# Kernel tuning notes

Hardware: AMD Instinct MI355X
Metric: run time of the kernel (lower is better)

## Reference

```python
import jax, jax.numpy as jnp
import numpy as np

DIM, EMBED, HEADS = 768, 512, 8
HEAD_DIM = EMBED // HEADS


def setup_inputs() -> dict:
    key = jax.random.key(0)
    ks = jax.random.split(key, 11)
    B, S = 4, 2048
    s = 0.02
    return {
        "query": jax.random.normal(ks[0], (B, S, DIM), jnp.float32),
        "key": jax.random.normal(ks[1], (B, S, DIM), jnp.float32),
        "value": jax.random.normal(ks[2], (B, S, DIM), jnp.float32),
        "wq": jax.random.normal(ks[3], (DIM, EMBED), jnp.float32) * s,
        "bq": jnp.zeros((EMBED,), jnp.float32),
        "wk": jax.random.normal(ks[4], (DIM, EMBED), jnp.float32) * s,
        "bk": jnp.zeros((EMBED,), jnp.float32),
        "wv": jax.random.normal(ks[5], (DIM, EMBED), jnp.float32) * s,
        "bv": jnp.zeros((EMBED,), jnp.float32),
        "wo": jax.random.normal(ks[6], (EMBED, DIM), jnp.float32) * s,
        "bo": jnp.zeros((DIM,), jnp.float32),
    }


def reference(query, key, value, wq, bq, wk, bk, wv, bv, wo, bo):
    B, S, _ = query.shape
    # QKV projections -> [B, H, S, Dh]
    def split_heads(x):
        return x.reshape(B, -1, HEADS, HEAD_DIM).transpose(0, 2, 1, 3)
    q = split_heads(query @ wq + bq)
    k = split_heads(key @ wk + bk)
    v = split_heads(value @ wv + bv)
    scores = jnp.einsum("bhqd,bhkd->bhqk", q, k) / jnp.sqrt(jnp.float32(HEAD_DIM))
    p = jax.nn.softmax(scores, axis=-1)
    x = jnp.einsum("bhqk,bhkd->bhqd", p, v)
    x = x.transpose(0, 2, 1, 3).reshape(B, S, EMBED)
    return x @ wo + bo
```

## Files before the change

### kernel.cpp

```cpp
#include <hip/hip_runtime.h>
#include <math.h>

#define NH   8
#define HD   64
#define BS   4
#define SEQL 2048
#define DIMX 768
#define EMB  512
#define MROWS (BS*SEQL)
#define NSPLIT 2
#define KSPAN (SEQL/NSPLIT)

typedef __attribute__((ext_vector_type(4))) float          f32x4;
typedef __attribute__((ext_vector_type(8))) __bf16         bf16x8;
typedef __attribute__((ext_vector_type(8))) unsigned short u16x8;
typedef __attribute__((ext_vector_type(4))) unsigned short u16x4;

union BF8 { u16x8 u; bf16x8 b; };

__device__ __forceinline__ unsigned short f2bf(float x) {
    unsigned int u = __float_as_uint(x);
    u += 0x7FFFu + ((u >> 16) & 1u);
    return (unsigned short)(u >> 16);
}

#if __has_builtin(__builtin_amdgcn_exp2f)
#define EXP2F(x) __builtin_amdgcn_exp2f(x)
#else
#define EXP2F(x) exp2f(x)
#endif

__device__ __forceinline__ bf16x8 ldb8(const unsigned short* p) {
    return *(const bf16x8*)p;
}

__global__ __launch_bounds__(256)
void cast3(const float* __restrict__ q, const float* __restrict__ k,
           const float* __restrict__ v, unsigned short* __restrict__ out)
{
    const float* src = blockIdx.y == 0 ? q : (blockIdx.y == 1 ? k : v);
    unsigned short* dst = out + (size_t)blockIdx.y * (MROWS * DIMX);
    const int n4 = MROWS * DIMX / 4;
    for (int i = blockIdx.x * 256 + threadIdx.x; i < n4; i += gridDim.x * 256) {
        f32x4 x = ((const f32x4*)src)[i];
        u16x4 o;
        o[0] = f2bf(x[0]); o[1] = f2bf(x[1]); o[2] = f2bf(x[2]); o[3] = f2bf(x[3]);
        ((u16x4*)dst)[i] = o;
    }
}

__global__ __launch_bounds__(256)
void transpose_w4(const float* __restrict__ w0, const float* __restrict__ w1,
                  const float* __restrict__ w2, const float* __restrict__ w3,
                  unsigned short* __restrict__ o0, unsigned short* __restrict__ o1,
                  unsigned short* __restrict__ o2, unsigned short* __restrict__ o3)
{
    __shared__ float sm[32][33];
    const int which = blockIdx.y;
    const float* in; unsigned short* out; int R, C;
    if      (which == 0) { in = w0; out = o0; R = DIMX; C = EMB;  }
    else if (which == 1) { in = w1; out = o1; R = DIMX; C = EMB;  }
    else if (which == 2) { in = w2; out = o2; R = DIMX; C = EMB;  }
    else                 { in = w3; out = o3; R = EMB;  C = DIMX; }
    const int nbx = C / 32;
    const int rB = (blockIdx.x / nbx) * 32, cB = (blockIdx.x % nbx) * 32;
    const int row = threadIdx.x >> 3, c4 = (threadIdx.x & 7) * 4;
    f32x4 v = *(const f32x4*)&in[(size_t)(rB + row) * C + cB + c4];
    sm[row][c4 + 0] = v[0]; sm[row][c4 + 1] = v[1];
    sm[row][c4 + 2] = v[2]; sm[row][c4 + 3] = v[3];
    __syncthreads();
    u16x4 o;
    o[0] = f2bf(sm[c4 + 0][row]); o[1] = f2bf(sm[c4 + 1][row]);
    o[2] = f2bf(sm[c4 + 2][row]); o[3] = f2bf(sm[c4 + 3][row]);
    *(u16x4*)&out[(size_t)(cB + row) * R + rB + c4] = o;
}

template<bool DIRECT>
__device__ __forceinline__ void gemm_core(
    const unsigned short* __restrict__ A, const unsigned short* __restrict__ Bt,
    int K, int mBase, int nBase,
    unsigned short* __restrict__ smA, unsigned short* __restrict__ smB,
    f32x4 (&acc)[4][4])
{
    const int tid = threadIdx.x;
    const int lane = tid & 63, w = tid >> 6;
    const int quad = lane >> 4, lanem = lane & 15;
    const int wm = w >> 1, wn = w & 1;
    const int srow = tid >> 3, c8 = (tid & 7) * 8;

    const f32x4 z4 = {0.f, 0.f, 0.f, 0.f};
    #pragma unroll
    for (int i = 0; i < 4; ++i)
        #pragma unroll
        for (int j = 0; j < 4; ++j) acc[i][j] = z4;

    for (int k0 = 0; k0 < K; k0 += 64) {
        u16x8 va[4], vb[4];
        #pragma unroll
        for (int p = 0; p < 4; ++p) {
            va[p] = *(const u16x8*)&A[(size_t)(mBase + srow + p * 32) * K + k0 + c8];
            vb[p] = *(const u16x8*)&Bt[(size_t)(nBase + srow + p * 32) * K + k0 + c8];
        }
        __syncthreads();
        #pragma unroll
        for (int p = 0; p < 4; ++p) {
            *(u16x8*)&smA[(srow + p * 32) * 72 + c8] = va[p];
            *(u16x8*)&smB[(srow + p * 32) * 72 + c8] = vb[p];
        }
        __syncthreads();
        #pragma unroll
        for (int kk = 0; kk < 64; kk += 32) {
            bf16x8 xa[4], wb[4];
            #pragma unroll
            for (int mt = 0; mt < 4; ++mt)
                xa[mt] = ldb8(&smA[(wm * 64 + mt * 16 + lanem) * 72 + kk + quad * 8]);
            #pragma unroll
            for (int nt = 0; nt < 4; ++nt)
                wb[nt] = ldb8(&smB[(wn * 64 + nt * 16 + lanem) * 72 + kk + quad * 8]);
            if constexpr (DIRECT) {
                #pragma unroll
                for (int mt = 0; mt < 4; ++mt)
                    #pragma unroll
                    for (int nt = 0; nt < 4; ++nt)
                        acc[mt][nt] = __builtin_amdgcn_mfma_f32_16x16x32_bf16(xa[mt], wb[nt], acc[mt][nt], 0, 0, 0);
            } else {
                #pragma unroll
                for (int nt = 0; nt < 4; ++nt)
                    #pragma unroll
                    for (int mt = 0; mt < 4; ++mt)
                        acc[nt][mt] = __builtin_amdgcn_mfma_f32_16x16x32_bf16(wb[nt], xa[mt], acc[nt][mt], 0, 0, 0);
            }
        }
    }
}

__global__ __launch_bounds__(256)
void gemm_qkv(const unsigned short* __restrict__ Xc, const unsigned short* __restrict__ Wt,
              const float* __restrict__ bq, const float* __restrict__ bk,
              const float* __restrict__ bv,
              unsigned short* __restrict__ Qb, unsigned short* __restrict__ Kb,
              unsigned short* __restrict__ Vtb)
{
    __shared__ unsigned short smA[128 * 72];
    __shared__ unsigned short smB[128 * 72];
    const int z = blockIdx.z;
    const unsigned short* A  = Xc + (size_t)z * (MROWS * DIMX);
    const unsigned short* Bt = Wt + (size_t)z * (EMB * DIMX);
    const float* bias = z == 0 ? bq : (z == 1 ? bk : bv);
    const int mBase = blockIdx.y * 128, nBase = blockIdx.x * 128;

    const int tid = threadIdx.x;
    const int lane = tid & 63, w = tid >> 6;
    const int quad = lane >> 4, lanem = lane & 15;
    const int wm = w >> 1, wn = w & 1;

    f32x4 acc[4][4];
    if (z == 2) {
        gemm_core<true>(A, Bt, DIMX, mBase, nBase, smA, smB, acc);
        #pragma unroll
        for (int mt = 0; mt < 4; ++mt) {
            const int sg = mBase + wm * 64 + mt * 16 + quad * 4;
            const int b = sg >> 11, s = sg & 2047;
            #pragma unroll
            for (int nt = 0; nt < 4; ++nt) {
                const int de = nBase + wn * 64 + nt * 16 + lanem;
                const float bvv = bias[de];
                const int h = de >> 6, dh = de & 63;
                u16x4 ov;
                #pragma unroll
                for (int r = 0; r < 4; ++r) ov[r] = f2bf(acc[mt][nt][r] + bvv);
                *(u16x4*)&Vtb[((size_t)((b * NH + h) * HD + dh) << 11) + s] = ov;
            }
        }
    } else {
        gemm_core<false>(A, Bt, DIMX, mBase, nBase, smA, smB, acc);
        const float os = (z == 0) ? 0.18033688f : 1.0f;
        unsigned short* C = (z == 0) ? Qb : Kb;
        #pragma unroll
        for (int nt = 0; nt < 4; ++nt) {
            const int n0 = nBase + wn * 64 + nt * 16 + quad * 4;
            const f32x4 b4 = *(const f32x4*)&bias[n0];
            #pragma unroll
            for (int mt = 0; mt < 4; ++mt) {
                const int m = mBase + wm * 64 + mt * 16 + lanem;
                u16x4 ov;
                #pragma unroll
                for (int r = 0; r < 4; ++r) ov[r] = f2bf((acc[nt][mt][r] + b4[r]) * os);
                *(u16x4*)&C[(size_t)m * EMB + n0] = ov;
            }
        }
    }
}

__global__ __launch_bounds__(256)
void gemm_out(const unsigned short* __restrict__ Xb, const unsigned short* __restrict__ Wot,
              const float* __restrict__ bo, float* __restrict__ out)
{
    __shared__ unsigned short smA[128 * 72];
    __shared__ unsigned short smB[128 * 72];
    const int mBase = blockIdx.y * 128, nBase = blockIdx.x * 128;
    const int tid = threadIdx.x;
    const int lane = tid & 63, w = tid >> 6;
    const int quad = lane >> 4, lanem = lane & 15;
    const int wm = w >> 1, wn = w & 1;

    f32x4 acc[4][4];
    gemm_core<false>(Xb, Wot, EMB, mBase, nBase, smA, smB, acc);
    #pragma unroll
    for (int nt = 0; nt < 4; ++nt) {
        const int n0 = nBase + wn * 64 + nt * 16 + quad * 4;
        const f32x4 b4 = *(const f32x4*)&bo[n0];
        #pragma unroll
        for (int mt = 0; mt < 4; ++mt) {
            const int m = mBase + wm * 64 + mt * 16 + lanem;
            f32x4 ov = acc[nt][mt] + b4;
            *(f32x4*)&out[(size_t)m * DIMX + n0] = ov;
        }
    }
}

__global__ __launch_bounds__(256)
void attn_mfma(const unsigned short* __restrict__ Qb, const unsigned short* __restrict__ Kb,
               const unsigned short* __restrict__ Vt,
               float* __restrict__ Opart, float* __restrict__ lpart)
{
    __shared__ unsigned short smK[64 * 72];
    __shared__ unsigned short smV[64 * 72];
    __shared__ unsigned short smP[4][32 * 72];
    const int id = blockIdx.x;
    const int bh = ((id & 7) << 2) | ((id >> 3) & 3);
    const int rest = id >> 5;
    const int qb = rest & 15, sp = rest >> 4;
    const int b = bh >> 3, h = bh & 7;

    const int tid = threadIdx.x;
    const int w = tid >> 6, lane = tid & 63;
    const int quad = lane >> 4, lanem = lane & 15;

    bf16x8 aq[2][2];
    #pragma unroll
    for (int rg = 0; rg < 2; ++rg) {
        const size_t qrow = (size_t)(b * SEQL + qb * 128 + w * 32 + rg * 16 + lanem) * EMB + h * HD;
        aq[rg][0] = ldb8(&Qb[qrow + quad * 8]);
        aq[rg][1] = ldb8(&Qb[qrow + 32 + quad * 8]);
    }

    const f32x4 z4 = {0.f, 0.f, 0.f, 0.f};
    f32x4 o[4][2];
    f32x4 ls[2] = {z4, z4};
    #pragma unroll
    for (int dt = 0; dt < 4; ++dt)
        #pragma unroll
        for (int rg = 0; rg < 2; ++rg) o[dt][rg] = z4;

    BF8 ones;
    #pragma unroll
    for (int i = 0; i < 8; ++i) ones.u[i] = 0x3F80;

    const unsigned short* Kbase = Kb + (size_t)b * SEQL * EMB + h * HD;
    const unsigned short* Vbase = Vt + (size_t)bh * HD * SEQL;
    unsigned short* pW = &smP[w][0];
    const int srow = tid >> 3, c8 = (tid & 7) * 8;

    for (int t = 0; t < KSPAN / 64; ++t) {
        const int k0 = sp * KSPAN + t * 64;
        u16x8 kv[2], vv[2];
        #pragma unroll
        for (int p = 0; p < 2; ++p) {
            kv[p] = *(const u16x8*)&Kbase[(size_t)(k0 + srow + p * 32) * EMB + c8];
            vv[p] = *(const u16x8*)&Vbase[(size_t)(srow + p * 32) * SEQL + k0 + c8];
        }
        __syncthreads();
        #pragma unroll
        for (int p = 0; p < 2; ++p) {
            *(u16x8*)&smK[(srow + p * 32) * 72 + c8] = kv[p];
            *(u16x8*)&smV[(srow + p * 32) * 72 + c8] = vv[p];
        }
        __syncthreads();

        #pragma unroll
        for (int nt = 0; nt < 4; ++nt) {
            bf16x8 bk0 = ldb8(&smK[(nt * 16 + lanem) * 72 + quad * 8]);
            bf16x8 bk1 = ldb8(&smK[(nt * 16 + lanem) * 72 + 32 + quad * 8]);
            #pragma unroll
            for (int rg = 0; rg < 2; ++rg) {
                f32x4 s = __builtin_amdgcn_mfma_f32_16x16x32_bf16(bk0, aq[rg][0], z4, 0, 0, 0);
                s = __builtin_amdgcn_mfma_f32_16x16x32_bf16(bk1, aq[rg][1], s, 0, 0, 0);
                u16x4 pk;
                #pragma unroll
                for (int r = 0; r < 4; ++r)
                    pk[r] = (unsigned short)(__float_as_uint(EXP2F(s[r])) >> 16);
                *(u16x4*)&pW[(rg * 16 + lanem) * 72 + nt * 16 + quad * 4] = pk;
            }
        }
        bf16x8 pb[2][2];
        #pragma unroll
        for (int rg = 0; rg < 2; ++rg) {
            pb[rg][0] = ldb8(&pW[(rg * 16 + lanem) * 72 + quad * 8]);
            pb[rg][1] = ldb8(&pW[(rg * 16 + lanem) * 72 + 32 + quad * 8]);
        }
        #pragma unroll
        for (int dt = 0; dt < 4; ++dt) {
            bf16x8 av0 = ldb8(&smV[(dt * 16 + lanem) * 72 + quad * 8]);
            bf16x8 av1 = ldb8(&smV[(dt * 16 + lanem) * 72 + 32 + quad * 8]);
            #pragma unroll
            for (int rg = 0; rg < 2; ++rg) {
                o[dt][rg] = __builtin_amdgcn_mfma_f32_16x16x32_bf16(av0, pb[rg][0], o[dt][rg], 0, 0, 0);
                o[dt][rg] = __builtin_amdgcn_mfma_f32_16x16x32_bf16(av1, pb[rg][1], o[dt][rg], 0, 0, 0);
            }
        }
        #pragma unroll
        for (int rg = 0; rg < 2; ++rg) {
            ls[rg] = __builtin_amdgcn_mfma_f32_16x16x32_bf16(ones.b, pb[rg][0], ls[rg], 0, 0, 0);
            ls[rg] = __builtin_amdgcn_mfma_f32_16x16x32_bf16(ones.b, pb[rg][1], ls[rg], 0, 0, 0);
        }
    }

    #pragma unroll
    for (int rg = 0; rg < 2; ++rg) {
        const int qloc = qb * 128 + w * 32 + rg * 16 + lanem;
        float* orow = Opart + ((size_t)sp * 32 * SEQL + (size_t)bh * SEQL + qloc) * HD;
        #pragma unroll
        for (int dt = 0; dt < 4; ++dt)
            *(f32x4*)&orow[dt * 16 + quad * 4] = o[dt][rg];
        if (quad == 0)
            lpart[(size_t)sp * 32 * SEQL + (size_t)bh * SEQL + qloc] = ls[rg][0];
    }
}

__global__ __launch_bounds__(256)
void attn_reduce(const float* __restrict__ Opart, const float* __restrict__ lpart,
                 unsigned short* __restrict__ Xb)
{
    const int lin = blockIdx.x * 256 + threadIdx.x;
    const int d4 = (lin & 15) << 2;
    const int q = (lin >> 4) & 2047;
    const int bh = lin >> 15;
    const int b = bh >> 3, h = bh & 7;
    const size_t base = ((size_t)bh * SEQL + q) * HD + d4;
    const size_t soff = (size_t)32 * SEQL * HD;
    f32x4 o0 = *(const f32x4*)&Opart[base];
    f32x4 o1 = *(const f32x4*)&Opart[base + soff];
    const float l0 = lpart[(size_t)bh * SEQL + q];
    const float l1 = lpart[(size_t)32 * SEQL + (size_t)bh * SEQL + q];
    const float rl = 1.f / (l0 + l1);
    u16x4 ov;
    #pragma unroll
    for (int r = 0; r < 4; ++r) ov[r] = f2bf((o0[r] + o1[r]) * rl);
    *(u16x4*)&Xb[((size_t)(b * SEQL + q)) * EMB + h * HD + d4] = ov;
}

extern "C" void kernel_launch(void* const* d_in, const int* in_sizes, int n_in,
                              void* d_out, int out_size, void* d_ws, size_t ws_size,
                              hipStream_t stream) {
    (void)in_sizes; (void)n_in; (void)out_size; (void)ws_size;
    const float* query = (const float*)d_in[0];
    const float* key   = (const float*)d_in[1];
    const float* value = (const float*)d_in[2];
    const float* wq = (const float*)d_in[3];
    const float* bq = (const float*)d_in[4];
    const float* wk = (const float*)d_in[5];
    const float* bk = (const float*)d_in[6];
    const float* wv = (const float*)d_in[7];
    const float* bv = (const float*)d_in[8];
    const float* wo = (const float*)d_in[9];
    const float* bo = (const float*)d_in[10];
    float* out = (float*)d_out;

    char* ws = (char*)d_ws;
    unsigned short* castb = (unsigned short*)(ws);
    float*          Opart = (float*)(ws);
    float*          lpart = (float*)(ws + 33554432);
    unsigned short* Wt    = (unsigned short*)(ws + 37748736);
    unsigned short* Wot   = (unsigned short*)(ws + 40108032);
    unsigned short* Qbuf  = (unsigned short*)(ws + 40894464);
    unsigned short* Xbuf  = Qbuf;
    unsigned short* Kbuf  = (unsigned short*)(ws + 49283072);
    unsigned short* Vtb   = (unsigned short*)(ws + 57671680);

    const dim3 blk(256);

    transpose_w4<<<dim3(384, 4), blk, 0, stream>>>(wq, wk, wv, wo,
        Wt, Wt + (size_t)EMB * DIMX, Wt + 2 * (size_t)EMB * DIMX, Wot);
    cast3<<<dim3(1024, 3), blk, 0, stream>>>(query, key, value, castb);

    gemm_qkv<<<dim3(EMB / 128, MROWS / 128, 3), blk, 0, stream>>>(
        castb, Wt, bq, bk, bv, Qbuf, Kbuf, Vtb);

    attn_mfma<<<dim3(32 * 16 * NSPLIT), blk, 0, stream>>>(Qbuf, Kbuf, Vtb, Opart, lpart);
    attn_reduce<<<dim3(4096), blk, 0, stream>>>(Opart, lpart, Xbuf);

    gemm_out<<<dim3(DIMX / 128, MROWS / 128), blk, 0, stream>>>(Xbuf, Wot, bo, out);
}
```

Baseline: 247.6 us.

## Fuse input cast into QKV GEMM, prefetch tiles, bf16 partials, 4-way KV split

Removes the separate fp32-to-bf16 cast kernel: the QKV GEMM now loads fp32 activations directly and packs them to bf16 by truncation with a byte-permute. The GEMM and attention loops register-prefetch the next tile while computing the current one. Attention partial outputs are stored as bf16 instead of fp32, and the KV split rises from 2 to 4 for more parallelism, with the reduce kernel summing all splits. Trade-offs are more register pressure, truncation instead of round-to-nearest on inputs, lower precision in the partial sums, and extra reduce traffic from the larger split.

Result: slower. 286.3 us (+15.6%).

```diff
diff --git a/kernel.cpp b/kernel.cpp
--- a/kernel.cpp
+++ b/kernel.cpp
@@ -8,7 +8,7 @@
 #define DIMX 768
 #define EMB  512
 #define MROWS (BS*SEQL)
-#define NSPLIT 2
+#define NSPLIT 4
 #define KSPAN (SEQL/NSPLIT)
 
 typedef __attribute__((ext_vector_type(4))) float          f32x4;
@@ -22,6 +22,10 @@
     unsigned int u = __float_as_uint(x);
     u += 0x7FFFu + ((u >> 16) & 1u);
     return (unsigned short)(u >> 16);
+}
+
+__device__ __forceinline__ unsigned int pktrunc(float a, float b) {
+    return __builtin_amdgcn_perm(__float_as_uint(b), __float_as_uint(a), 0x07060302);
 }
 
 #if __has_builtin(__builtin_amdgcn_exp2f)
@@ -32,21 +36,6 @@
 
 __device__ __forceinline__ bf16x8 ldb8(const unsigned short* p) {
     return *(const bf16x8*)p;
-}
-
-__global__ __launch_bounds__(256)
-void cast3(const float* __restrict__ q, const float* __restrict__ k,
-           const float* __restrict__ v, unsigned short* __restrict__ out)
-{
-    const float* src = blockIdx.y == 0 ? q : (blockIdx.y == 1 ? k : v);
-    unsigned short* dst = out + (size_t)blockIdx.y * (MROWS * DIMX);
-    const int n4 = MROWS * DIMX / 4;
-    for (int i = blockIdx.x * 256 + threadIdx.x; i < n4; i += gridDim.x * 256) {
-        f32x4 x = ((const f32x4*)src)[i];
-        u16x4 o;
-        o[0] = f2bf(x[0]); o[1] = f2bf(x[1]); o[2] = f2bf(x[2]); o[3] = f2bf(x[3]);
-        ((u16x4*)dst)[i] = o;
-    }
 }
 
 __global__ __launch_bounds__(256)
@@ -75,9 +64,9 @@
     *(u16x4*)&out[(size_t)(cB + row) * R + rB + c4] = o;
 }
 
-template<bool DIRECT>
+template<bool DIRECT, bool AF32>
 __device__ __forceinline__ void gemm_core(
-    const unsigned short* __restrict__ A, const unsigned short* __restrict__ Bt,
+    const void* __restrict__ Av, const unsigned short* __restrict__ Bt,
     int K, int mBase, int nBase,
     unsigned short* __restrict__ smA, unsigned short* __restrict__ smB,
     f32x4 (&acc)[4][4])
@@ -87,6 +76,8 @@
     const int quad = lane >> 4, lanem = lane & 15;
     const int wm = w >> 1, wn = w & 1;
     const int srow = tid >> 3, c8 = (tid & 7) * 8;
+    const unsigned short* Ab = (const unsigned short*)Av;
+    const float* Af = (const float*)Av;
 
     const f32x4 z4 = {0.f, 0.f, 0.f, 0.f};
     #pragma unroll
@@ -94,13 +85,30 @@
         #pragma unroll
         for (int j = 0; j < 4; ++j) acc[i][j] = z4;
 
+    auto ldA = [&](int p, int k0) -> u16x8 {
+        if constexpr (AF32) {
+            const float* bp = &Af[(size_t)(mBase + srow + p * 32) * K + k0 + c8];
+            f32x4 x0 = *(const f32x4*)bp;
+            f32x4 x1 = *(const f32x4*)(bp + 4);
+            union { unsigned int d[4]; u16x8 u; } t;
+            t.d[0] = pktrunc(x0[0], x0[1]);
+            t.d[1] = pktrunc(x0[2], x0[3]);
+            t.d[2] = pktrunc(x1[0], x1[1]);
+            t.d[3] = pktrunc(x1[2], x1[3]);
+            return t.u;
+        } else {
+            return *(const u16x8*)&Ab[(size_t)(mBase + srow + p * 32) * K + k0 + c8];
+        }
+    };
+    auto ldB = [&](int p, int k0) -> u16x8 {
+        return *(const u16x8*)&Bt[(size_t)(nBase + srow + p * 32) * K + k0 + c8];
+    };
+
+    u16x8 va[4], vb[4];
+    #pragma unroll
+    for (int p = 0; p < 4; ++p) { va[p] = ldA(p, 0); vb[p] = ldB(p, 0); }
+
     for (int k0 = 0; k0 < K; k0 += 64) {
-        u16x8 va[4], vb[4];
-        #pragma unroll
-        for (int p = 0; p < 4; ++p) {
-            va[p] = *(const u16x8*)&A[(size_t)(mBase + srow + p * 32) * K + k0 + c8];
-            vb[p] = *(const u16x8*)&Bt[(size_t)(nBase + srow + p * 32) * K + k0 + c8];
-        }
         __syncthreads();
         #pragma unroll
         for (int p = 0; p < 4; ++p) {
@@ -108,6 +116,10 @@
             *(u16x8*)&smB[(srow + p * 32) * 72 + c8] = vb[p];
         }
         __syncthreads();
+        const int kn = (k0 + 64 < K) ? k0 + 64 : 0;
+        #pragma unroll
+        for (int p = 0; p < 4; ++p) { va[p] = ldA(p, kn); vb[p] = ldB(p, kn); }
+
         #pragma unroll
         for (int kk = 0; kk < 64; kk += 32) {
             bf16x8 xa[4], wb[4];
@@ -135,7 +147,8 @@
 }
 
 __global__ __launch_bounds__(256)
-void gemm_qkv(const unsigned short* __restrict__ Xc, const unsigned short* __restrict__ Wt,
+void gemm_qkv(const float* __restrict__ query, const float* __restrict__ keyt,
+              const float* __restrict__ value, const unsigned short* __restrict__ Wt,
               const float* __restrict__ bq, const float* __restrict__ bk,
               const float* __restrict__ bv,
               unsigned short* __restrict__ Qb, unsigned short* __restrict__ Kb,
@@ -144,7 +157,7 @@
     __shared__ unsigned short smA[128 * 72];
     __shared__ unsigned short smB[128 * 72];
     const int z = blockIdx.z;
-    const unsigned short* A  = Xc + (size_t)z * (MROWS * DIMX);
+    const float* A = z == 0 ? query : (z == 1 ? keyt : value);
     const unsigned short* Bt = Wt + (size_t)z * (EMB * DIMX);
     const float* bias = z == 0 ? bq : (z == 1 ? bk : bv);
     const int mBase = blockIdx.y * 128, nBase = blockIdx.x * 128;
@@ -156,7 +169,7 @@
 
     f32x4 acc[4][4];
     if (z == 2) {
-        gemm_core<true>(A, Bt, DIMX, mBase, nBase, smA, smB, acc);
+        gemm_core<true, true>(A, Bt, DIMX, mBase, nBase, smA, smB, acc);
         #pragma unroll
         for (int mt = 0; mt < 4; ++mt) {
             const int sg = mBase + wm * 64 + mt * 16 + quad * 4;
@@ -173,7 +186,7 @@
             }
         }
     } else {
-        gemm_core<false>(A, Bt, DIMX, mBase, nBase, smA, smB, acc);
+        gemm_core<false, true>(A, Bt, DIMX, mBase, nBase, smA, smB, acc);
         const float os = (z == 0) ? 0.18033688f : 1.0f;
         unsigned short* C = (z == 0) ? Qb : Kb;
         #pragma unroll
@@ -205,7 +218,7 @@
     const int wm = w >> 1, wn = w & 1;
 
     f32x4 acc[4][4];
-    gemm_core<false>(Xb, Wot, EMB, mBase, nBase, smA, smB, acc);
+    gemm_core<false, false>(Xb, Wot, EMB, mBase, nBase, smA, smB, acc);
     #pragma unroll
     for (int nt = 0; nt < 4; ++nt) {
         const int n0 = nBase + wn * 64 + nt * 16 + quad * 4;
@@ -222,7 +235,7 @@
 __global__ __launch_bounds__(256)
 void attn_mfma(const unsigned short* __restrict__ Qb, const unsigned short* __restrict__ Kb,
                const unsigned short* __restrict__ Vt,
-               float* __restrict__ Opart, float* __restrict__ lpart)
+               unsigned short* __restrict__ Opart, float* __restrict__ lpart)
 {
     __shared__ unsigned short smK[64 * 72];
     __shared__ unsigned short smV[64 * 72];
@@ -262,14 +275,14 @@
     unsigned short* pW = &smP[w][0];
     const int srow = tid >> 3, c8 = (tid & 7) * 8;
 
+    u16x8 kv[2], vv[2];
+    #pragma unroll
+    for (int p = 0; p < 2; ++p) {
+        kv[p] = *(const u16x8*)&Kbase[(size_t)(sp * KSPAN + srow + p * 32) * EMB + c8];
+        vv[p] = *(const u16x8*)&Vbase[(size_t)(srow + p * 32) * SEQL + sp * KSPAN + c8];
+    }
+
     for (int t = 0; t < KSPAN / 64; ++t) {
-        const int k0 = sp * KSPAN + t * 64;
-        u16x8 kv[2], vv[2];
-        #pragma unroll
-        for (int p = 0; p < 2; ++p) {
-            kv[p] = *(const u16x8*)&Kbase[(size_t)(k0 + srow + p * 32) * EMB + c8];
-            vv[p] = *(const u16x8*)&Vbase[(size_t)(srow + p * 32) * SEQL + k0 + c8];
-        }
         __syncthreads();
         #pragma unroll
         for (int p = 0; p < 2; ++p) {
@@ -277,6 +290,12 @@
             *(u16x8*)&smV[(srow + p * 32) * 72 + c8] = vv[p];
         }
         __syncthreads();
+        const int k1 = (t + 1 < KSPAN / 64) ? sp * KSPAN + (t + 1) * 64 : sp * KSPAN;
+        #pragma unroll
+        for (int p = 0; p < 2; ++p) {
+            kv[p] = *(const u16x8*)&Kbase[(size_t)(k1 + srow + p * 32) * EMB + c8];
+            vv[p] = *(const u16x8*)&Vbase[(size_t)(srow + p * 32) * SEQL + k1 + c8];
+        }
 
         #pragma unroll
         for (int nt = 0; nt < 4; ++nt) {
@@ -319,17 +338,22 @@
     #pragma unroll
     for (int rg = 0; rg < 2; ++rg) {
         const int qloc = qb * 128 + w * 32 + rg * 16 + lanem;
-        float* orow = Opart + ((size_t)sp * 32 * SEQL + (size_t)bh * SEQL + qloc) * HD;
-        #pragma unroll
-        for (int dt = 0; dt < 4; ++dt)
-            *(f32x4*)&orow[dt * 16 + quad * 4] = o[dt][rg];
+        unsigned short* orow =
+            Opart + ((size_t)sp * 32 * SEQL + (size_t)bh * SEQL + qloc) * HD;
+        #pragma unroll
+        for (int dt = 0; dt < 4; ++dt) {
+            u16x4 ov;
+            #pragma unroll
+            for (int r = 0; r < 4; ++r) ov[r] = f2bf(o[dt][rg][r]);
+            *(u16x4*)&orow[dt * 16 + quad * 4] = ov;
+        }
         if (quad == 0)
             lpart[(size_t)sp * 32 * SEQL + (size_t)bh * SEQL + qloc] = ls[rg][0];
     }
 }
 
 __global__ __launch_bounds__(256)
-void attn_reduce(const float* __restrict__ Opart, const float* __restrict__ lpart,
+void attn_reduce(const unsigned short* __restrict__ Opart, const float* __restrict__ lpart,
                  unsigned short* __restrict__ Xb)
 {
     const int lin = blockIdx.x * 256 + threadIdx.x;
@@ -339,15 +363,23 @@
     const int b = bh >> 3, h = bh & 7;
     const size_t base = ((size_t)bh * SEQL + q) * HD + d4;
     const size_t soff = (size_t)32 * SEQL * HD;
-    f32x4 o0 = *(const f32x4*)&Opart[base];
-    f32x4 o1 = *(const f32x4*)&Opart[base + soff];
-    const float l0 = lpart[(size_t)bh * SEQL + q];
-    const float l1 = lpart[(size_t)32 * SEQL + (size_t)bh * SEQL + q];
-    const float rl = 1.f / (l0 + l1);
-    u16x4 ov;
-    #pragma unroll
-    for (int r = 0; r < 4; ++r) ov[r] = f2bf((o0[r] + o1[r]) * rl);
-    *(u16x4*)&Xb[((size_t)(b * SEQL + q)) * EMB + h * HD + d4] = ov;
+    const size_t lbase = (size_t)bh * SEQL + q;
+    const size_t lstr = (size_t)32 * SEQL;
+    float acc[4] = {0.f, 0.f, 0.f, 0.f};
+    float l = 0.f;
+    #pragma unroll
+    for (int sp = 0; sp < NSPLIT; ++sp) {
+        u16x4 ov = *(const u16x4*)&Opart[base + (size_t)sp * soff];
+        #pragma unroll
+        for (int r = 0; r < 4; ++r)
+            acc[r] += __uint_as_float((unsigned int)ov[r] << 16);
+        l += lpart[lbase + (size_t)sp * lstr];
+    }
+    const float rl = 1.f / l;
+    u16x4 xo;
+    #pragma unroll
+    for (int r = 0; r < 4; ++r) xo[r] = f2bf(acc[r] * rl);
+    *(u16x4*)&Xb[((size_t)(b * SEQL + q)) * EMB + h * HD + d4] = xo;
 }
 
 extern "C" void kernel_launch(void* const* d_in, const int* in_sizes, int n_in,
@@ -368,24 +400,22 @@
     float* out = (float*)d_out;
 
     char* ws = (char*)d_ws;
-    unsigned short* castb = (unsigned short*)(ws);
-    float*          Opart = (float*)(ws);
+    unsigned short* Opart = (unsigned short*)(ws);
     float*          lpart = (float*)(ws + 33554432);
-    unsigned short* Wt    = (unsigned short*)(ws + 37748736);
-    unsigned short* Wot   = (unsigned short*)(ws + 40108032);
-    unsigned short* Qbuf  = (unsigned short*)(ws + 40894464);
+    unsigned short* Wt    = (unsigned short*)(ws + 35651584);
+    unsigned short* Wot   = (unsigned short*)(ws + 38010880);
+    unsigned short* Qbuf  = (unsigned short*)(ws + 38797312);
     unsigned short* Xbuf  = Qbuf;
-    unsigned short* Kbuf  = (unsigned short*)(ws + 49283072);
-    unsigned short* Vtb   = (unsigned short*)(ws + 57671680);
+    unsigned short* Kbuf  = (unsigned short*)(ws + 47185920);
+    unsigned short* Vtb   = (unsigned short*)(ws + 55574528);
 
     const dim3 blk(256);
 
     transpose_w4<<<dim3(384, 4), blk, 0, stream>>>(wq, wk, wv, wo,
         Wt, Wt + (size_t)EMB * DIMX, Wt + 2 * (size_t)EMB * DIMX, Wot);
-    cast3<<<dim3(1024, 3), blk, 0, stream>>>(query, key, value, castb);
 
     gemm_qkv<<<dim3(EMB / 128, MROWS / 128, 3), blk, 0, stream>>>(
-        castb, Wt, bq, bk, bv, Qbuf, Kbuf, Vtb);
+        query, key, value, Wt, bq, bk, bv, Qbuf, Kbuf, Vtb);
 
     attn_mfma<<<dim3(32 * 16 * NSPLIT), blk, 0, stream>>>(Qbuf, Kbuf, Vtb, Opart, lpart);
     attn_reduce<<<dim3(4096), blk, 0, stream>>>(Opart, lpart, Xbuf);
```
